# Kernel optimization log

Hardware: AMD Instinct MI355X
Metric: run time of the kernel (lower is better)

Reference implementation:

```python
import jax, jax.numpy as jnp
import numpy as np

B, C, H, W = 2, 256, 64, 64
NUM_HEADS = 4
HEAD_DIM = C // NUM_HEADS
N = H * W


def setup_inputs() -> dict:
    key = jax.random.key(0)
    ks = jax.random.split(key, 10)
    x = jax.random.normal(ks[0], (B, C, H, W), dtype=jnp.float32)
    # mostly-True mask; diagonal forced True so every row has a valid key
    m = jax.random.uniform(ks[1], (B, N, N)) > 0.1
    spatial_mask = m | jnp.eye(N, dtype=bool)[None]
    s = 1.0 / np.sqrt(C)
    wq = jax.random.normal(ks[2], (C, C), dtype=jnp.float32) * s
    bq = jnp.zeros((C,), jnp.float32)
    wk = jax.random.normal(ks[3], (C, C), dtype=jnp.float32) * s
    bk = jnp.zeros((C,), jnp.float32)
    wv = jax.random.normal(ks[4], (C, C), dtype=jnp.float32) * s
    bv = jnp.zeros((C,), jnp.float32)
    # torch zero-inits out_proj; use random weights for a non-trivial baseline
    wo = jax.random.normal(ks[5], (C, C), dtype=jnp.float32) * s
    bo = jnp.zeros((C,), jnp.float32)
    return {"x": x, "spatial_mask": spatial_mask, "wq": wq, "bq": bq,
            "wk": wk, "bk": bk, "wv": wv, "bv": bv, "wo": wo, "bo": bo}


def reference(x, spatial_mask, wq, bq, wk, bk, wv, bv, wo, bo):
    b, c, h, w = x.shape
    n = h * w
    nh, hd = NUM_HEADS, HEAD_DIM
    scale = hd ** -0.5
    x_flat = x.reshape(b, c, n).transpose(0, 2, 1)           # [b, n, c]
    q = (x_flat @ wq.T + bq).reshape(b, n, nh, hd).transpose(0, 2, 1, 3)
    k = (x_flat @ wk.T + bk).reshape(b, n, nh, hd).transpose(0, 2, 1, 3)
    v = (x_flat @ wv.T + bv).reshape(b, n, nh, hd).transpose(0, 2, 1, 3)
    logits = jnp.einsum('bhqd,bhkd->bhqk', q, k) * scale      # [b, nh, n, n]
    logits = jnp.where(spatial_mask[:, None], logits, -jnp.inf)
    attn = jax.nn.softmax(logits, axis=-1)                    # dropout = identity (eval)
    out = jnp.einsum('bhqk,bhkd->bhqd', attn, v)              # [b, nh, n, hd]
    out = out.transpose(0, 2, 1, 3).reshape(b, n, c)
    out = out @ wo.T + bo
    return out.transpose(0, 2, 1).reshape(b, c, h, w)
```

## Files before the change

### kernel.cpp

```cpp
#include <hip/hip_runtime.h>
#include <math.h>

namespace {
constexpr int B_    = 2;
constexpr int C_    = 256;
constexpr int NHEAD = 4;
constexpr int HDIM  = 64;
constexpr int NTOK  = 4096;
constexpr float SCALE = 0.125f;
constexpr float LOG2E = 1.44269504f;
}

typedef _Float16 half8  __attribute__((ext_vector_type(8)));
typedef _Float16 half4  __attribute__((ext_vector_type(4)));
typedef __fp16   fp16x2 __attribute__((ext_vector_type(2)));
typedef float    floatx4 __attribute__((ext_vector_type(4)));
typedef int      int4v   __attribute__((ext_vector_type(4)));
typedef unsigned int uint2v __attribute__((ext_vector_type(2)));

__device__ __forceinline__ void plswap32(int &a, int &b) {
#if __has_builtin(__builtin_amdgcn_permlane32_swap)
    const uint2v r = __builtin_amdgcn_permlane32_swap((unsigned)a, (unsigned)b, false, false);
    a = (int)r[0]; b = (int)r[1];
#else
    asm volatile("s_nop 1\n\tv_permlane32_swap_b32 %0, %1\n\ts_nop 1"
                 : "+v"(a), "+v"(b));
#endif
}
__device__ __forceinline__ void plswap16(int &a, int &b) {
#if __has_builtin(__builtin_amdgcn_permlane16_swap)
    const uint2v r = __builtin_amdgcn_permlane16_swap((unsigned)a, (unsigned)b, false, false);
    a = (int)r[0]; b = (int)r[1];
#else
    asm volatile("s_nop 1\n\tv_permlane16_swap_b32 %0, %1\n\ts_nop 1"
                 : "+v"(a), "+v"(b));
#endif
}

__device__ __forceinline__ void gload_lds16(const _Float16* g, _Float16* l, int lane) {
#if __has_builtin(__builtin_amdgcn_global_load_lds)
    __builtin_amdgcn_global_load_lds(
        (const __attribute__((address_space(1))) void*)g,
        (__attribute__((address_space(3))) void*)l, 16, 0, 0);
#else
    *(half8*)((char*)l + lane * 16) = *(const half8*)g;
#endif
}

__global__ __launch_bounds__(256) void wprep(
    const float* __restrict__ wq, const float* __restrict__ wk,
    const float* __restrict__ wv, const float* __restrict__ wo,
    _Float16* __restrict__ w16)
{
    const float* src = (blockIdx.y == 0) ? wq :
                       (blockIdx.y == 1) ? wk :
                       (blockIdx.y == 2) ? wv : wo;
    const int i8 = (blockIdx.x * 256 + threadIdx.x) * 8;
    const float4 a = *(const float4*)&src[i8];
    const float4 b = *(const float4*)&src[i8 + 4];
    half8 h;
    h[0]=(_Float16)a.x; h[1]=(_Float16)a.y; h[2]=(_Float16)a.z; h[3]=(_Float16)a.w;
    h[4]=(_Float16)b.x; h[5]=(_Float16)b.y; h[6]=(_Float16)b.z; h[7]=(_Float16)b.w;
    *(half8*)&w16[(size_t)blockIdx.y * 65536 + i8] = h;
}

__global__ __launch_bounds__(256) void pack_mask(
    const unsigned int* __restrict__ m32, unsigned int* __restrict__ packed)
{
    int c0 = 0, c1 = 0, c2 = 0, c3 = 0;
    #pragma unroll
    for (int i = 0; i < 16; i++) {
        const unsigned int d = m32[i];
        c0 += (d == 0x00000001u);
        c1 += (d == 0x3F803F80u);
        c2 += (d == 0x3F800000u);
        c3 += (d == 0x01010101u);
    }
    int fmt = 1, best = c1;
    if (c0 > best) { best = c0; fmt = 0; }
    if (c2 > best) { best = c2; fmt = 2; }
    if (c3 > best) { best = c3; fmt = 3; }

    const unsigned int W = blockIdx.x * 256 + threadIdx.x;
    unsigned int bits = 0;
    if (fmt == 1) {
        const uint4* p4 = (const uint4*)(m32 + (size_t)W * 16);
        #pragma unroll
        for (int i = 0; i < 4; i++) {
            const uint4 v = p4[i];
            const unsigned int d[4] = { v.x, v.y, v.z, v.w };
            #pragma unroll
            for (int j = 0; j < 4; j++) {
                const int e = i * 8 + j * 2;
                bits |= ((d[j] & 0xFFFFu) ? 1u : 0u) << e;
                bits |= ((d[j] >> 16)     ? 1u : 0u) << (e + 1);
            }
        }
    } else if (fmt != 3) {
        const uint4* p4 = (const uint4*)(m32 + (size_t)W * 32);
        #pragma unroll
        for (int i = 0; i < 8; i++) {
            const uint4 v = p4[i];
            bits |= (v.x ? 1u : 0u) << (i * 4 + 0);
            bits |= (v.y ? 1u : 0u) << (i * 4 + 1);
            bits |= (v.z ? 1u : 0u) << (i * 4 + 2);
            bits |= (v.w ? 1u : 0u) << (i * 4 + 3);
        }
    } else {
        const uint4* p4 = (const uint4*)(m32 + (size_t)W * 8);
        #pragma unroll
        for (int i = 0; i < 2; i++) {
            const uint4 v = p4[i];
            const unsigned int d[4] = { v.x, v.y, v.z, v.w };
            #pragma unroll
            for (int j = 0; j < 4; j++) {
                const int e = (i * 4 + j) * 4;
                bits |= ((d[j] & 0x000000FFu) ? 1u : 0u) << (e + 0);
                bits |= ((d[j] & 0x0000FF00u) ? 1u : 0u) << (e + 1);
                bits |= ((d[j] & 0x00FF0000u) ? 1u : 0u) << (e + 2);
                bits |= ((d[j] & 0xFF000000u) ? 1u : 0u) << (e + 3);
            }
        }
    }
    packed[W] = bits;
}

__global__ __launch_bounds__(256) void qkv_mfma(
    const float* __restrict__ x, const _Float16* __restrict__ w16,
    const float* __restrict__ bq, const float* __restrict__ bk,
    const float* __restrict__ bv,
    _Float16* __restrict__ qo, _Float16* __restrict__ ko,
    _Float16* __restrict__ vo)
{
    const int nt = blockIdx.x;
    const int b  = blockIdx.y;
    const int p  = blockIdx.z;

    const _Float16* w = w16 + (size_t)p * C_ * C_;
    const float* bias = (p == 0) ? bq : (p == 1) ? bk : bv;

    const int t    = threadIdx.x;
    const int wid  = t >> 6;
    const int lane = t & 63;
    const int quad = lane >> 4;
    const int l15  = lane & 15;
    const int n0   = nt * 64;

    __shared__ _Float16 xsh[64 * 264];
    __shared__ _Float16 tbuf[64 * 72];

    const int srow = t >> 2;
    const int sc   = (t & 3) * 16;

    {
        const int cr = t >> 4;
        const int nu = (t & 15) * 4;
        const float* xb = x + (size_t)b * C_ * NTOK;
        #pragma unroll
        for (int cc = 0; cc < 16; cc++) {
            const int cl = cc * 16 + cr;
            const float4 v = *(const float4*)&xb[(size_t)cl * NTOK + n0 + nu];
            xsh[(nu + 0) * 264 + cl] = (_Float16)v.x;
            xsh[(nu + 1) * 264 + cl] = (_Float16)v.y;
            xsh[(nu + 2) * 264 + cl] = (_Float16)v.z;
            xsh[(nu + 3) * 264 + cl] = (_Float16)v.w;
        }
    }
    __syncthreads();

    const _Float16* wrow = &w[(size_t)(wid * 16 + l15) * C_];

    for (int h = 0; h < NHEAD; h++) {
        const int co0 = h * 64;
        floatx4 acc[4];
        #pragma unroll
        for (int i = 0; i < 4; i++) acc[i] = (floatx4)0.f;

        #pragma unroll
        for (int c0 = 0; c0 < C_; c0 += 64) {
            const half8 a0 = *(const half8*)&wrow[(size_t)co0 * C_ + c0 + quad * 8];
            const half8 a1 = *(const half8*)&wrow[(size_t)co0 * C_ + c0 + 32 + quad * 8];
            #pragma unroll
            for (int nt2 = 0; nt2 < 4; nt2++) {
                const half8 b0 = *(const half8*)&xsh[(nt2 * 16 + l15) * 264 + c0 + quad * 8];
                const half8 b1 = *(const half8*)&xsh[(nt2 * 16 + l15) * 264 + c0 + 32 + quad * 8];
                acc[nt2] = __builtin_amdgcn_mfma_f32_16x16x32_f16(a0, b0, acc[nt2], 0, 0, 0);
                acc[nt2] = __builtin_amdgcn_mfma_f32_16x16x32_f16(a1, b1, acc[nt2], 0, 0, 0);
            }
        }

        const float4 bb4 = *(const float4*)&bias[co0 + wid * 16 + quad * 4];
        const float bb[4] = { bb4.x, bb4.y, bb4.z, bb4.w };

        if (p < 2) {
            const float osc = (p == 0) ? (SCALE * LOG2E) : 1.0f;
            #pragma unroll
            for (int nt2 = 0; nt2 < 4; nt2++) {
                half4 hv;
                #pragma unroll
                for (int i = 0; i < 4; i++)
                    hv[i] = (_Float16)((acc[nt2][i] + bb[i]) * osc);
                *(half4*)&tbuf[(nt2 * 16 + l15) * 72 + wid * 16 + quad * 4] = hv;
            }
            __syncthreads();
            _Float16* dh = (p == 0 ? qo : ko) + (size_t)(b * NHEAD + h) * NTOK * HDIM;
            const half8 o0 = *(const half8*)&tbuf[srow * 72 + sc];
            const half8 o1 = *(const half8*)&tbuf[srow * 72 + sc + 8];
            *(half8*)&dh[(size_t)(n0 + srow) * HDIM + sc]     = o0;
            *(half8*)&dh[(size_t)(n0 + srow) * HDIM + sc + 8] = o1;
        } else {
            #pragma unroll
            for (int nt2 = 0; nt2 < 4; nt2++)
                #pragma unroll
                for (int i = 0; i < 4; i++)
                    tbuf[(wid * 16 + quad * 4 + i) * 72 + nt2 * 16 + l15] =
                        (_Float16)(acc[nt2][i] + bb[i]);
            __syncthreads();
            _Float16* vth = vo + (size_t)(b * NHEAD + h) * HDIM * NTOK;
            const half8 o0 = *(const half8*)&tbuf[srow * 72 + sc];
            const half8 o1 = *(const half8*)&tbuf[srow * 72 + sc + 8];
            *(half8*)&vth[(size_t)srow * NTOK + n0 + sc]     = o0;
            *(half8*)&vth[(size_t)srow * NTOK + n0 + sc + 8] = o1;
        }
        __syncthreads();
    }
}

__global__ __launch_bounds__(512) void attn(
    const _Float16* __restrict__ q, const _Float16* __restrict__ k,
    const _Float16* __restrict__ vt, const unsigned int* __restrict__ mpacked,
    _Float16* __restrict__ ao)
{
    const int b  = blockIdx.z;
    const int h  = blockIdx.y;
    const int q0 = blockIdx.x * 64;
    const int t    = threadIdx.x;
    const int w    = t >> 6;
    const int lane = t & 63;
    const int quad = lane >> 4;
    const int l15  = lane & 15;
    const int half = w >> 2;
    const int w4   = w & 3;
    const int koff = half * (NTOK / 2);

    __shared__ __align__(16) char smem_raw[65536];
    _Float16* const sbase = (_Float16*)(smem_raw + half * 32768);

    const size_t head_off = (size_t)(b * NHEAD + h) * NTOK * HDIM;
    const _Float16* qb  = q  + head_off;
    const _Float16* kb  = k  + head_off;
    const _Float16* vtb = vt + head_off;
    const unsigned int* mrow = mpacked + (size_t)b * NTOK * 128;

    const int qrow = q0 + w4 * 16 + l15;
    half8 aq0 = *(const half8*)&qb[(size_t)qrow * HDIM + quad * 8];
    half8 aq1 = *(const half8*)&qb[(size_t)qrow * HDIM + 32 + quad * 8];
    const unsigned int* mq = &mrow[(size_t)qrow * 128];

    const int jr  = l15 & 7;
    const int xs0 = (quad ^ jr) << 3;
    const int xs1 = ((quad + 4) ^ jr) << 3;

    uint2 mw = *(const uint2*)&mq[koff >> 5];
    uint2 mw_nxt = mw;

    float l_loc = 0.f;
    floatx4 o_acc[4];
    #pragma unroll
    for (int i = 0; i < 4; i++) o_acc[i] = (floatx4)0.f;

#define STAGE(WO, K0N)                                                        \
    {                                                                         \
        const int rl = lane >> 3;                       \
        const int xc = ((lane & 7) ^ rl) << 3;        \
        const int c0 = w4 * 2, c1 = c0 + 1;                                   \
        gload_lds16(&kb[(size_t)((K0N) + c0 * 8 + rl) * HDIM + xc],           \
                    &sbase[(WO) + c0 * 512], lane);                           \
        gload_lds16(&kb[(size_t)((K0N) + c1 * 8 + rl) * HDIM + xc],           \
                    &sbase[(WO) + c1 * 512], lane);                           \
        gload_lds16(&vtb[(size_t)(c0 * 8 + rl) * NTOK + (K0N) + xc],          \
                    &sbase[(WO) + 4096 + c0 * 512], lane);                    \
        gload_lds16(&vtb[(size_t)(c1 * 8 + rl) * NTOK + (K0N) + xc],          \
                    &sbase[(WO) + 4096 + c1 * 512], lane);                    \
    }

    STAGE(0, koff)
    __syncthreads();

#define SOFTMAX_CT(CT, WORD, SH, Pa, Pb)                                          \
    {                                                                             \
        const unsigned nib = ((WORD) >> ((SH) + quad * 4)) & 0xFu;                \
        const float p0 = __builtin_amdgcn_exp2f((nib & 1u) ? sa[CT][0] : -3.0e38f);\
        const float p1 = __builtin_amdgcn_exp2f((nib & 2u) ? sa[CT][1] : -3.0e38f);\
        const float p2 = __builtin_amdgcn_exp2f((nib & 4u) ? sa[CT][2] : -3.0e38f);\
        const float p3 = __builtin_amdgcn_exp2f((nib & 8u) ? sa[CT][3] : -3.0e38f);\
        l_loc += (p0 + p1) + (p2 + p3);                                           \
        Pa = __builtin_bit_cast(int, __builtin_amdgcn_cvt_pkrtz(p0, p1));         \
        Pb = __builtin_bit_cast(int, __builtin_amdgcn_cvt_pkrtz(p2, p3));         \
    }

#define ATTN_TILE(RO, WO, KT, PF)                                                 \
    {                                                                             \
        if (PF) {                                                                 \
            const int k0n = koff + (KT) * 64 + 64;                                \
            STAGE(WO, k0n)                                                        \
            mw_nxt = *(const uint2*)&mq[k0n >> 5];                                \
        }                                                                         \
        floatx4 sa[4];                                                            \
        __builtin_amdgcn_s_setprio(1);                                            \
        _Pragma("unroll")                                                         \
        for (int ct = 0; ct < 4; ct++) {                                          \
            sa[ct] = (floatx4)0.f;                                                \
            const half8 ka0 = *(const half8*)&sbase[(RO) + (ct*16 + l15)*64 + xs0];\
            const half8 ka1 = *(const half8*)&sbase[(RO) + (ct*16 + l15)*64 + xs1];\
            sa[ct] = __builtin_amdgcn_mfma_f32_16x16x32_f16(ka0, aq0, sa[ct], 0, 0, 0);     \
            sa[ct] = __builtin_amdgcn_mfma_f32_16x16x32_f16(ka1, aq1, sa[ct], 0, 0, 0);     \
        }                                                                         \
        __builtin_amdgcn_s_setprio(0);                                            \
        int P00, P01, P10, P11, P20, P21, P30, P31;                               \
        SOFTMAX_CT(0, mw.x, 0,  P00, P01)                                         \
        SOFTMAX_CT(1, mw.x, 16, P10, P11)                                         \
        SOFTMAX_CT(2, mw.y, 0,  P20, P21)                                         \
        SOFTMAX_CT(3, mw.y, 16, P30, P31)                                         \
        mw = mw_nxt;                                                              \
        plswap32(P00, P10); plswap32(P01, P11);                                   \
        plswap32(P20, P30); plswap32(P21, P31);                                   \
        plswap16(P00, P10); plswap16(P01, P11);                                   \
        plswap16(P20, P30); plswap16(P21, P31);                                   \
        const half8 pb0 = __builtin_bit_cast(half8, (int4v){P00, P01, P10, P11}); \
        const half8 pb1 = __builtin_bit_cast(half8, (int4v){P20, P21, P30, P31}); \
        __builtin_amdgcn_s_setprio(1);                                            \
        _Pragma("unroll")                                                         \
        for (int dt = 0; dt < 4; dt++) {                                          \
            const half8 va0 = *(const half8*)&sbase[(RO) + 4096 + (dt*16 + l15)*64 + xs0];\
            const half8 va1 = *(const half8*)&sbase[(RO) + 4096 + (dt*16 + l15)*64 + xs1];\
            o_acc[dt] = __builtin_amdgcn_mfma_f32_16x16x32_f16(va0, pb0, o_acc[dt], 0, 0, 0);      \
            o_acc[dt] = __builtin_amdgcn_mfma_f32_16x16x32_f16(va1, pb1, o_acc[dt], 0, 0, 0);      \
        }                                                                         \
        __builtin_amdgcn_s_setprio(0);                                            \
        __syncthreads();                                                          \
    }

    for (int kt2 = 0; kt2 < 15; kt2++) {
        ATTN_TILE(0,    8192, 2 * kt2,     1)
        ATTN_TILE(8192, 0,    2 * kt2 + 1, 1)
    }
    ATTN_TILE(0,    8192, 30, 1)
    ATTN_TILE(8192, 0,    31, 0)

#undef ATTN_TILE
#undef SOFTMAX_CT
#undef STAGE

    l_loc += __shfl_xor(l_loc, 16, 64);
    l_loc += __shfl_xor(l_loc, 32, 64);

    float* oex = (float*)smem_raw;
    float* lex = (float*)(smem_raw + 16384);
    if (w >= 4) {
        float* dst = &oex[((size_t)(w - 4) * 64 + lane) * 16];
        #pragma unroll
        for (int dt = 0; dt < 4; dt++)
            *(floatx4*)&dst[dt * 4] = o_acc[dt];
        if (quad == 0) lex[(w - 4) * 16 + l15] = l_loc;
    }
    __syncthreads();
    if (w < 4) {
        const float* src = &oex[((size_t)w * 64 + lane) * 16];
        const float lt = l_loc + lex[w * 16 + l15];
        const float inv = (lt > 0.f) ? (1.0f / lt) : 0.f;
        _Float16* aob = ao + ((size_t)b * NTOK + q0 + w * 16 + l15) * C_ + h * 64;
        #pragma unroll
        for (int dt = 0; dt < 4; dt++) {
            const floatx4 o2 = *(const floatx4*)&src[dt * 4];
            half4 r;
            #pragma unroll
            for (int rr = 0; rr < 4; rr++)
                r[rr] = (_Float16)((o_acc[dt][rr] + o2[rr]) * inv);
            *(half4*)&aob[dt * 16 + quad * 4] = r;
        }
    }
}

__global__ __launch_bounds__(256) void out_mfma(
    const _Float16* __restrict__ ao, const _Float16* __restrict__ wo16,
    const float* __restrict__ bo, float* __restrict__ out)
{
    const int nt  = blockIdx.x;
    const int cot = blockIdx.y;
    const int b   = blockIdx.z;
    const int t    = threadIdx.x;
    const int wid  = t >> 6;
    const int lane = t & 63;
    const int quad = lane >> 4;
    const int l15  = lane & 15;
    const int n0  = nt * 64;
    const int co0 = cot * 64;

    __shared__ float tf[64 * 68];

    floatx4 acc[4];
    #pragma unroll
    for (int i = 0; i < 4; i++) acc[i] = (floatx4)0.f;

    const _Float16* wrow = &wo16[(size_t)(co0 + wid * 16 + l15) * C_];
    const _Float16* aob  = ao + ((size_t)b * NTOK + n0) * C_;

    #pragma unroll
    for (int c0 = 0; c0 < C_; c0 += 64) {
        const half8 a0 = *(const half8*)&wrow[c0 + quad * 8];
        const half8 a1 = *(const half8*)&wrow[c0 + 32 + quad * 8];
        #pragma unroll
        for (int nt2 = 0; nt2 < 4; nt2++) {
            const half8 b0 = *(const half8*)&aob[(size_t)(nt2 * 16 + l15) * C_ + c0 + quad * 8];
            const half8 b1 = *(const half8*)&aob[(size_t)(nt2 * 16 + l15) * C_ + c0 + 32 + quad * 8];
            acc[nt2] = __builtin_amdgcn_mfma_f32_16x16x32_f16(a0, b0, acc[nt2], 0, 0, 0);
            acc[nt2] = __builtin_amdgcn_mfma_f32_16x16x32_f16(a1, b1, acc[nt2], 0, 0, 0);
        }
    }

    #pragma unroll
    for (int nt2 = 0; nt2 < 4; nt2++)
        #pragma unroll
        for (int i = 0; i < 4; i++)
            tf[(wid * 16 + quad * 4 + i) * 68 + nt2 * 16 + l15] = acc[nt2][i];
    __syncthreads();

    const int row = t >> 2;
    const int c4  = (t & 3) * 16;
    const float bb = bo[co0 + row];
    float* orow = &out[((size_t)(b * C_ + co0 + row)) * NTOK + n0 + c4];
    #pragma unroll
    for (int u = 0; u < 4; u++) {
        float4 v = *(const float4*)&tf[row * 68 + c4 + u * 4];
        v.x += bb; v.y += bb; v.z += bb; v.w += bb;
        *(float4*)&orow[u * 4] = v;
    }
}

extern "C" void kernel_launch(void* const* d_in, const int* in_sizes, int n_in,
                              void* d_out, int out_size, void* d_ws, size_t ws_size,
                              hipStream_t stream) {
    const float* x    = (const float*)d_in[0];
    const void*  mask = d_in[1];
    const float* wq   = (const float*)d_in[2];
    const float* bq   = (const float*)d_in[3];
    const float* wk   = (const float*)d_in[4];
    const float* bk   = (const float*)d_in[5];
    const float* wv   = (const float*)d_in[6];
    const float* bv   = (const float*)d_in[7];
    const float* wo   = (const float*)d_in[8];
    const float* bo   = (const float*)d_in[9];
    float* out = (float*)d_out;

    const size_t qkv_elems = (size_t)B_ * NHEAD * NTOK * HDIM;
    _Float16* wsh = (_Float16*)d_ws;
    _Float16* qbuf  = wsh;
    _Float16* kbuf  = wsh + qkv_elems;
    _Float16* vtbuf = wsh + 2 * qkv_elems;
    _Float16* aobuf = wsh + 3 * qkv_elems;
    unsigned int* mpacked = (unsigned int*)(wsh + 4 * qkv_elems);
    _Float16* w16buf = wsh + 4 * qkv_elems + 2 * (size_t)(B_ * NTOK * 128);

    wprep<<<dim3(32, 4), 256, 0, stream>>>(wq, wk, wv, wo, w16buf);
    pack_mask<<<dim3((B_ * NTOK * 128) / 256), 256, 0, stream>>>(
        (const unsigned int*)mask, mpacked);
    qkv_mfma<<<dim3(NTOK / 64, B_, 3), 256, 0, stream>>>(
        x, w16buf, bq, bk, bv, qbuf, kbuf, vtbuf);
    attn<<<dim3(NTOK / 64, NHEAD, B_), 512, 0, stream>>>(
        qbuf, kbuf, vtbuf, mpacked, aobuf);
    out_mfma<<<dim3(NTOK / 64, C_ / 64, B_), 256, 0, stream>>>(
        aobuf, w16buf + 3 * 65536, bo, out);
}
```

Before: 293.8 us.

## Process two 64-row query tiles per attention block to reuse staged K/V

Each attention block now handles 128 query rows instead of 64, with every wave computing two 16-row query groups against the same K/V tiles in shared memory. This halves global K/V loads and staging per query row and doubles MFMA work per LDS read. In exchange it uses more registers for the second set of accumulators and score tiles, and launches half as many blocks (256), which may lower occupancy on the GPU. The cross-half reduction buffer is enlarged, and a barrier is added before reusing shared memory.

```diff
diff --git a/kernel.cpp b/kernel.cpp
--- a/kernel.cpp
+++ b/kernel.cpp
@@ -233,7 +233,7 @@
 {
     const int b  = blockIdx.z;
     const int h  = blockIdx.y;
-    const int q0 = blockIdx.x * 64;
+    const int q0 = blockIdx.x * 128;
     const int t    = threadIdx.x;
     const int w    = t >> 6;
     const int lane = t & 63;
@@ -252,22 +252,27 @@
     const _Float16* vtb = vt + head_off;
     const unsigned int* mrow = mpacked + (size_t)b * NTOK * 128;
 
-    const int qrow = q0 + w4 * 16 + l15;
-    half8 aq0 = *(const half8*)&qb[(size_t)qrow * HDIM + quad * 8];
-    half8 aq1 = *(const half8*)&qb[(size_t)qrow * HDIM + 32 + quad * 8];
-    const unsigned int* mq = &mrow[(size_t)qrow * 128];
+    const int qrowa = q0 + w4 * 16 + l15;
+    const int qrowb = qrowa + 64;
+    const half8 aq0a = *(const half8*)&qb[(size_t)qrowa * HDIM + quad * 8];
+    const half8 aq1a = *(const half8*)&qb[(size_t)qrowa * HDIM + 32 + quad * 8];
+    const half8 aq0b = *(const half8*)&qb[(size_t)qrowb * HDIM + quad * 8];
+    const half8 aq1b = *(const half8*)&qb[(size_t)qrowb * HDIM + 32 + quad * 8];
+    const unsigned int* mqa = &mrow[(size_t)qrowa * 128];
+    const unsigned int* mqb = &mrow[(size_t)qrowb * 128];
 
     const int jr  = l15 & 7;
     const int xs0 = (quad ^ jr) << 3;
     const int xs1 = ((quad + 4) ^ jr) << 3;
 
-    uint2 mw = *(const uint2*)&mq[koff >> 5];
-    uint2 mw_nxt = mw;
-
-    float l_loc = 0.f;
-    floatx4 o_acc[4];
+    uint2 mwa = *(const uint2*)&mqa[koff >> 5];
+    uint2 mwb = *(const uint2*)&mqb[koff >> 5];
+    uint2 mwa_nxt = mwa, mwb_nxt = mwb;
+
+    float l_a = 0.f, l_b = 0.f;
+    floatx4 oacca[4], oaccb[4];
     #pragma unroll
-    for (int i = 0; i < 4; i++) o_acc[i] = (floatx4)0.f;
+    for (int i = 0; i < 4; i++) { oacca[i] = (floatx4)0.f; oaccb[i] = (floatx4)0.f; }
 
 #define STAGE(WO, K0N)                                                        \
     {                                                                         \
@@ -287,14 +292,14 @@
     STAGE(0, koff)
     __syncthreads();
 
-#define SOFTMAX_CT(CT, WORD, SH, Pa, Pb)                                          \
+#define SOFTMAX_CT(SA, CT, WORD, SH, LL, Pa, Pb)                                  \
     {                                                                             \
         const unsigned nib = ((WORD) >> ((SH) + quad * 4)) & 0xFu;                \
-        const float p0 = __builtin_amdgcn_exp2f((nib & 1u) ? sa[CT][0] : -3.0e38f);\
-        const float p1 = __builtin_amdgcn_exp2f((nib & 2u) ? sa[CT][1] : -3.0e38f);\
-        const float p2 = __builtin_amdgcn_exp2f((nib & 4u) ? sa[CT][2] : -3.0e38f);\
-        const float p3 = __builtin_amdgcn_exp2f((nib & 8u) ? sa[CT][3] : -3.0e38f);\
-        l_loc += (p0 + p1) + (p2 + p3);                                           \
+        const float p0 = __builtin_amdgcn_exp2f((nib & 1u) ? SA[CT][0] : -3.0e38f);\
+        const float p1 = __builtin_amdgcn_exp2f((nib & 2u) ? SA[CT][1] : -3.0e38f);\
+        const float p2 = __builtin_amdgcn_exp2f((nib & 4u) ? SA[CT][2] : -3.0e38f);\
+        const float p3 = __builtin_amdgcn_exp2f((nib & 8u) ? SA[CT][3] : -3.0e38f);\
+        LL += (p0 + p1) + (p2 + p3);                                              \
         Pa = __builtin_bit_cast(int, __builtin_amdgcn_cvt_pkrtz(p0, p1));         \
         Pb = __builtin_bit_cast(int, __builtin_amdgcn_cvt_pkrtz(p2, p3));         \
     }
@@ -304,38 +309,54 @@
         if (PF) {                                                                 \
             const int k0n = koff + (KT) * 64 + 64;                                \
             STAGE(WO, k0n)                                                        \
-            mw_nxt = *(const uint2*)&mq[k0n >> 5];                                \
+            mwa_nxt = *(const uint2*)&mqa[k0n >> 5];                              \
+            mwb_nxt = *(const uint2*)&mqb[k0n >> 5];                              \
         }                                                                         \
-        floatx4 sa[4];                                                            \
+        floatx4 saa[4], sab[4];                                                   \
         __builtin_amdgcn_s_setprio(1);                                            \
         _Pragma("unroll")                                                         \
         for (int ct = 0; ct < 4; ct++) {                                          \
-            sa[ct] = (floatx4)0.f;                                                \
+            saa[ct] = (floatx4)0.f; sab[ct] = (floatx4)0.f;                       \
             const half8 ka0 = *(const half8*)&sbase[(RO) + (ct*16 + l15)*64 + xs0];\
             const half8 ka1 = *(const half8*)&sbase[(RO) + (ct*16 + l15)*64 + xs1];\
-            sa[ct] = __builtin_amdgcn_mfma_f32_16x16x32_f16(ka0, aq0, sa[ct], 0, 0, 0);     \
-            sa[ct] = __builtin_amdgcn_mfma_f32_16x16x32_f16(ka1, aq1, sa[ct], 0, 0, 0);     \
+            saa[ct] = __builtin_amdgcn_mfma_f32_16x16x32_f16(ka0, aq0a, saa[ct], 0, 0, 0); \
+            saa[ct] = __builtin_amdgcn_mfma_f32_16x16x32_f16(ka1, aq1a, saa[ct], 0, 0, 0); \
+            sab[ct] = __builtin_amdgcn_mfma_f32_16x16x32_f16(ka0, aq0b, sab[ct], 0, 0, 0); \
+            sab[ct] = __builtin_amdgcn_mfma_f32_16x16x32_f16(ka1, aq1b, sab[ct], 0, 0, 0); \
         }                                                                         \
         __builtin_amdgcn_s_setprio(0);                                            \
-        int P00, P01, P10, P11, P20, P21, P30, P31;                               \
-        SOFTMAX_CT(0, mw.x, 0,  P00, P01)                                         \
-        SOFTMAX_CT(1, mw.x, 16, P10, P11)                                         \
-        SOFTMAX_CT(2, mw.y, 0,  P20, P21)                                         \
-        SOFTMAX_CT(3, mw.y, 16, P30, P31)                                         \
-        mw = mw_nxt;                                                              \
-        plswap32(P00, P10); plswap32(P01, P11);                                   \
-        plswap32(P20, P30); plswap32(P21, P31);                                   \
-        plswap16(P00, P10); plswap16(P01, P11);                                   \
-        plswap16(P20, P30); plswap16(P21, P31);                                   \
-        const half8 pb0 = __builtin_bit_cast(half8, (int4v){P00, P01, P10, P11}); \
-        const half8 pb1 = __builtin_bit_cast(half8, (int4v){P20, P21, P30, P31}); \
+        int A00,A01,A10,A11,A20,A21,A30,A31;                                      \
+        int B00,B01,B10,B11,B20,B21,B30,B31;                                      \
+        SOFTMAX_CT(saa, 0, mwa.x, 0,  l_a, A00, A01)                              \
+        SOFTMAX_CT(saa, 1, mwa.x, 16, l_a, A10, A11)                              \
+        SOFTMAX_CT(saa, 2, mwa.y, 0,  l_a, A20, A21)                              \
+        SOFTMAX_CT(saa, 3, mwa.y, 16, l_a, A30, A31)                              \
+        SOFTMAX_CT(sab, 0, mwb.x, 0,  l_b, B00, B01)                              \
+        SOFTMAX_CT(sab, 1, mwb.x, 16, l_b, B10, B11)                              \
+        SOFTMAX_CT(sab, 2, mwb.y, 0,  l_b, B20, B21)                              \
+        SOFTMAX_CT(sab, 3, mwb.y, 16, l_b, B30, B31)                              \
+        mwa = mwa_nxt; mwb = mwb_nxt;                                             \
+        plswap32(A00, A10); plswap32(A01, A11);                                   \
+        plswap32(A20, A30); plswap32(A21, A31);                                   \
+        plswap16(A00, A10); plswap16(A01, A11);                                   \
+        plswap16(A20, A30); plswap16(A21, A31);                                   \
+        plswap32(B00, B10); plswap32(B01, B11);                                   \
+        plswap32(B20, B30); plswap32(B21, B31);                                   \
+        plswap16(B00, B10); plswap16(B01, B11);                                   \
+        plswap16(B20, B30); plswap16(B21, B31);                                   \
+        const half8 pb0a = __builtin_bit_cast(half8, (int4v){A00, A01, A10, A11});\
+        const half8 pb1a = __builtin_bit_cast(half8, (int4v){A20, A21, A30, A31});\
+        const half8 pb0b = __builtin_bit_cast(half8, (int4v){B00, B01, B10, B11});\
+        const half8 pb1b = __builtin_bit_cast(half8, (int4v){B20, B21, B30, B31});\
         __builtin_amdgcn_s_setprio(1);                                            \
         _Pragma("unroll")                                                         \
         for (int dt = 0; dt < 4; dt++) {                                          \
             const half8 va0 = *(const half8*)&sbase[(RO) + 4096 + (dt*16 + l15)*64 + xs0];\
             const half8 va1 = *(const half8*)&sbase[(RO) + 4096 + (dt*16 + l15)*64 + xs1];\
-            o_acc[dt] = __builtin_amdgcn_mfma_f32_16x16x32_f16(va0, pb0, o_acc[dt], 0, 0, 0);      \
-            o_acc[dt] = __builtin_amdgcn_mfma_f32_16x16x32_f16(va1, pb1, o_acc[dt], 0, 0, 0);      \
+            oacca[dt] = __builtin_amdgcn_mfma_f32_16x16x32_f16(va0, pb0a, oacca[dt], 0, 0, 0); \
+            oacca[dt] = __builtin_amdgcn_mfma_f32_16x16x32_f16(va1, pb1a, oacca[dt], 0, 0, 0); \
+            oaccb[dt] = __builtin_amdgcn_mfma_f32_16x16x32_f16(va0, pb0b, oaccb[dt], 0, 0, 0); \
+            oaccb[dt] = __builtin_amdgcn_mfma_f32_16x16x32_f16(va1, pb1b, oaccb[dt], 0, 0, 0); \
         }                                                                         \
         __builtin_amdgcn_s_setprio(0);                                            \
         __syncthreads();                                                          \
@@ -352,32 +373,47 @@
 #undef SOFTMAX_CT
 #undef STAGE
 
-    l_loc += __shfl_xor(l_loc, 16, 64);
-    l_loc += __shfl_xor(l_loc, 32, 64);
-
+    l_a += __shfl_xor(l_a, 16, 64);
+    l_a += __shfl_xor(l_a, 32, 64);
+    l_b += __shfl_xor(l_b, 16, 64);
+    l_b += __shfl_xor(l_b, 32, 64);
+
+    __syncthreads();
     float* oex = (float*)smem_raw;
-    float* lex = (float*)(smem_raw + 16384);
+    float* lex = (float*)(smem_raw + 32768);
     if (w >= 4) {
-        float* dst = &oex[((size_t)(w - 4) * 64 + lane) * 16];
-        #pragma unroll
-        for (int dt = 0; dt < 4; dt++)
-            *(floatx4*)&dst[dt * 4] = o_acc[dt];
-        if (quad == 0) lex[(w - 4) * 16 + l15] = l_loc;
+        float* dst = &oex[((size_t)(w - 4) * 64 + lane) * 32];
+        #pragma unroll
+        for (int dt = 0; dt < 4; dt++) {
+            *(floatx4*)&dst[dt * 4]      = oacca[dt];
+            *(floatx4*)&dst[16 + dt * 4] = oaccb[dt];
+        }
+        if (quad == 0) {
+            lex[(w - 4) * 16 + l15]      = l_a;
+            lex[64 + (w - 4) * 16 + l15] = l_b;
+        }
     }
     __syncthreads();
     if (w < 4) {
-        const float* src = &oex[((size_t)w * 64 + lane) * 16];
-        const float lt = l_loc + lex[w * 16 + l15];
-        const float inv = (lt > 0.f) ? (1.0f / lt) : 0.f;
-        _Float16* aob = ao + ((size_t)b * NTOK + q0 + w * 16 + l15) * C_ + h * 64;
+        const float* src = &oex[((size_t)w * 64 + lane) * 32];
+        const float lta = l_a + lex[w * 16 + l15];
+        const float ltb = l_b + lex[64 + w * 16 + l15];
+        const float inva = (lta > 0.f) ? (1.0f / lta) : 0.f;
+        const float invb = (ltb > 0.f) ? (1.0f / ltb) : 0.f;
+        _Float16* aoba = ao + ((size_t)b * NTOK + q0 + w * 16 + l15) * C_ + h * 64;
+        _Float16* aobb = ao + ((size_t)b * NTOK + q0 + 64 + w * 16 + l15) * C_ + h * 64;
         #pragma unroll
         for (int dt = 0; dt < 4; dt++) {
-            const floatx4 o2 = *(const floatx4*)&src[dt * 4];
-            half4 r;
+            const floatx4 o2a = *(const floatx4*)&src[dt * 4];
+            const floatx4 o2b = *(const floatx4*)&src[16 + dt * 4];
+            half4 ra, rb;
             #pragma unroll
-            for (int rr = 0; rr < 4; rr++)
-                r[rr] = (_Float16)((o_acc[dt][rr] + o2[rr]) * inv);
-            *(half4*)&aob[dt * 16 + quad * 4] = r;
+            for (int rr = 0; rr < 4; rr++) {
+                ra[rr] = (_Float16)((oacca[dt][rr] + o2a[rr]) * inva);
+                rb[rr] = (_Float16)((oaccb[dt][rr] + o2b[rr]) * invb);
+            }
+            *(half4*)&aoba[dt * 16 + quad * 4] = ra;
+            *(half4*)&aobb[dt * 16 + quad * 4] = rb;
         }
     }
 }
@@ -467,7 +503,7 @@
         (const unsigned int*)mask, mpacked);
     qkv_mfma<<<dim3(NTOK / 64, B_, 3), 256, 0, stream>>>(
         x, w16buf, bq, bk, bv, qbuf, kbuf, vtbuf);
-    attn<<<dim3(NTOK / 64, NHEAD, B_), 512, 0, stream>>>(
+    attn<<<dim3(NTOK / 128, NHEAD, B_), 512, 0, stream>>>(
         qbuf, kbuf, vtbuf, mpacked, aobuf);
     out_mfma<<<dim3(NTOK / 64, C_ / 64, B_), 256, 0, stream>>>(
         aobuf, w16buf + 3 * 65536, bo, out);
```

Result: no change. 292.1 us (-0.6%).
